# Performance work log

Measured on AMD Instinct MI355X. Metric: run time of the kernel, lower is better.

Reference implementation:

```python
import jax, jax.numpy as jnp
import numpy as np

N = 50000
E = 800000
EMB = 128
HID = 128
HALF = HID // 2

def setup_inputs() -> dict:
    key = jax.random.key(0)
    ks = jax.random.split(key, 16)
    inp = {
        "x": jax.random.normal(ks[0], (N, EMB), dtype=jnp.float32),
        "edge_row": jax.random.randint(ks[1], (E,), 0, N, dtype=jnp.int32),
        "edge_col": jax.random.randint(ks[2], (E,), 0, N, dtype=jnp.int32),
        "edge_vals": jax.random.uniform(ks[3], (E,), dtype=jnp.float32),
        "W_gc0": jax.random.normal(ks[4], (EMB, HID), dtype=jnp.float32) * 0.05,
        "b_gc0": jax.random.normal(ks[5], (HID,), dtype=jnp.float32) * 0.05,
        "W_gc1": jax.random.normal(ks[6], (HID, HID), dtype=jnp.float32) * 0.05,
        "b_gc1": jax.random.normal(ks[7], (HID,), dtype=jnp.float32) * 0.05,
        "Wm1": jax.random.normal(ks[8], (HID, HALF), dtype=jnp.float32) * 0.05,
        "bm1": jax.random.normal(ks[9], (HALF,), dtype=jnp.float32) * 0.05,
        "Wm2": jax.random.normal(ks[10], (HALF, HALF), dtype=jnp.float32) * 0.05,
        "bm2": jax.random.normal(ks[11], (HALF,), dtype=jnp.float32) * 0.05,
        "Wv1": jax.random.normal(ks[12], (HID, HALF), dtype=jnp.float32) * 0.05,
        "bv1": jax.random.normal(ks[13], (HALF,), dtype=jnp.float32) * 0.05,
        "Wv2": jax.random.normal(ks[14], (HALF, HALF), dtype=jnp.float32) * 0.05,
        "bv2": jax.random.normal(ks[15], (HALF,), dtype=jnp.float32) * 0.05,
    }
    return inp

def reference(x, edge_row, edge_col, edge_vals,
              W_gc0, b_gc0, W_gc1, b_gc1,
              Wm1, bm1, Wm2, bm2, Wv1, bv1, Wv2, bv2):
    n = x.shape[0]

    def gcn_layer(h, W, b):
        # support = h @ W  (dense GEMM), then spmm: out[r] += adj[r,c] * support[c]
        support = h @ W                                   # [N, out]
        msgs = edge_vals[:, None] * support[edge_col]      # [E, out]
        agg = jax.ops.segment_sum(msgs, edge_row, num_segments=n)
        return agg + b

    h = jax.nn.relu(gcn_layer(x, W_gc0, b_gc0))
    h = jax.nn.relu(gcn_layer(h, W_gc1, b_gc1))

    mean = jax.nn.relu(h @ Wm1 + bm1) @ Wm2 + bm2
    logvar = jax.nn.relu(h @ Wv1 + bv1) @ Wv2 + bv2
    return mean, logvar
```

## Files before the change

kernel.cpp:

```cpp
#include <hip/hip_runtime.h>
#include <type_traits>


typedef _Float16 half8 __attribute__((ext_vector_type(8)));
typedef float floatx4 __attribute__((ext_vector_type(4)));

#define BCAP 2560
#define CHUNK 2048
#define RB 128

template<int K, int M, bool RELU, bool BIAS2, bool SPLIT, typename InT, typename OutT>
__global__ __launch_bounds__(256)
void gemm16(const InT* __restrict__ A, const _Float16* __restrict__ Wswz,
            const float* __restrict__ bias0, const float* __restrict__ bias1,
            OutT* __restrict__ C0, OutT* __restrict__ C1, int n) {
  constexpr int NT = M / 16, KS = K / 32;
  const int lane = threadIdx.x & 63;
  const int wave = threadIdx.x >> 6;
  const int quad = lane >> 4, l16 = lane & 15;
  const int r_base = blockIdx.x * 128 + wave * 32;

  int arow0 = r_base + l16;
  int arow1 = r_base + 16 + l16;
  if (arow0 >= n) arow0 = n - 1;
  if (arow1 >= n) arow1 = n - 1;
  const InT* Ap0 = A + (size_t)arow0 * K + quad * 8;
  const InT* Ap1 = A + (size_t)arow1 * K + quad * 8;

  floatx4 acc[2][NT] = {};

#pragma unroll
  for (int ks = 0; ks < KS; ++ks) {
    half8 a0, a1;
    if constexpr (std::is_same_v<InT, _Float16>) {
      a0 = *(const half8*)(Ap0 + ks * 32);
      a1 = *(const half8*)(Ap1 + ks * 32);
    } else {
      float4 u = *(const float4*)(Ap0 + ks * 32);
      float4 w = *(const float4*)(Ap0 + ks * 32 + 4);
      a0 = half8{(_Float16)u.x, (_Float16)u.y, (_Float16)u.z, (_Float16)u.w,
                 (_Float16)w.x, (_Float16)w.y, (_Float16)w.z, (_Float16)w.w};
      float4 u1 = *(const float4*)(Ap1 + ks * 32);
      float4 w1 = *(const float4*)(Ap1 + ks * 32 + 4);
      a1 = half8{(_Float16)u1.x, (_Float16)u1.y, (_Float16)u1.z, (_Float16)u1.w,
                 (_Float16)w1.x, (_Float16)w1.y, (_Float16)w1.z, (_Float16)w1.w};
    }
#pragma unroll
    for (int nt = 0; nt < NT; ++nt) {
      half8 b = *(const half8*)(Wswz + ((size_t)(ks * NT + nt) * 64 + lane) * 8);
      acc[0][nt] = __builtin_amdgcn_mfma_f32_16x16x32_f16(a0, b, acc[0][nt], 0, 0, 0);
      acc[1][nt] = __builtin_amdgcn_mfma_f32_16x16x32_f16(a1, b, acc[1][nt], 0, 0, 0);
    }
  }

#pragma unroll
  for (int h = 0; h < 2; ++h) {
#pragma unroll
    for (int nt = 0; nt < NT; ++nt) {
      const int col = nt * 16 + l16;
      float bv = 0.f;
      if constexpr (BIAS2) bv = (col < 64) ? bias0[col] : bias1[col - 64];
#pragma unroll
      for (int r = 0; r < 4; ++r) {
        int row = r_base + h * 16 + quad * 4 + r;
        if (row < n) {
          float v = acc[h][nt][r] + bv;
          if constexpr (RELU) v = fmaxf(v, 0.f);
          if constexpr (SPLIT) {
            if (col < 64) C0[(size_t)row * 64 + col] = (OutT)v;
            else          C1[(size_t)row * 64 + (col - 64)] = (OutT)v;
          } else {
            C0[(size_t)row * M + col] = (OutT)v;
          }
        }
      }
    }
  }
}

__global__ __launch_bounds__(256)
void wconv_kernel(const float* __restrict__ w0, const float* __restrict__ w1,
                  const float* __restrict__ wm1, const float* __restrict__ wv1,
                  const float* __restrict__ wm2, const float* __restrict__ wv2,
                  _Float16* __restrict__ d0, _Float16* __restrict__ d1,
                  _Float16* __restrict__ dh1, _Float16* __restrict__ dh2) {
  int i = blockIdx.x * 256 + threadIdx.x;
  if (i >= 65536) return;
  int seg = i >> 14, li = i & 16383;
  int j = li & 7, lane = (li >> 3) & 63, t = li >> 9;
  int nt = t & 7, ks = t >> 3;
  int k = ks * 32 + (lane >> 4) * 8 + j;
  int n = nt * 16 + (lane & 15);
  float v;
  if (seg == 0)      v = w0[k * 128 + n];
  else if (seg == 1) v = w1[k * 128 + n];
  else if (seg == 2) v = (n < 64) ? wm1[k * 64 + n] : wv1[k * 64 + (n - 64)];
  else v = (k < 64 && n < 64) ? wm2[k * 64 + n]
         : (k >= 64 && n >= 64) ? wv2[(k - 64) * 64 + (n - 64)] : 0.f;
  _Float16* dst = (seg == 0) ? d0 : (seg == 1) ? d1 : (seg == 2) ? dh1 : dh2;
  dst[li] = (_Float16)v;
}

__global__ __launch_bounds__(256)
void blockbin_kernel(const int* __restrict__ rows, const int* __restrict__ cols,
                     const float* __restrict__ vals,
                     int* __restrict__ bcur, uint2* __restrict__ bbuf, int e) {
  __shared__ int cnt[392];
  __shared__ int cur[392];
  const int t = threadIdx.x;
  const int lo = blockIdx.x * CHUNK, hi = min(lo + CHUNK, e);
  for (int j = t; j < 392; j += 256) cnt[j] = 0;
  __syncthreads();
  for (int i = lo + t; i < hi; i += 256)
    atomicAdd(&cnt[rows[i] >> 7], 1);
  __syncthreads();
  for (int j = t; j < 392; j += 256)
    if (cnt[j] > 0) cur[j] = atomicAdd(&bcur[j * 16], cnt[j]);
  __syncthreads();
  for (int i = lo + t; i < hi; i += 256) {
    int r = rows[i];
    int b = r >> 7;
    int p = atomicAdd(&cur[b], 1);
    if (p < BCAP)
      bbuf[(size_t)b * BCAP + p] =
          make_uint2(((unsigned)(r & (RB - 1)) << 16) | (unsigned)cols[i],
                     __float_as_uint(vals[i]));
  }
}

__global__ __launch_bounds__(512)
void bscan_kernel(const int* __restrict__ bcur, int* __restrict__ bbase,
                  int* __restrict__ row_ptr, int nbk, int n) {
  __shared__ int s[512];
  int t = threadIdx.x;
  int c = (t < nbk) ? bcur[t * 16] : 0;
  s[t] = c;
  __syncthreads();
#pragma unroll
  for (int off = 1; off < 512; off <<= 1) {
    int a = (t >= off) ? s[t - off] : 0;
    __syncthreads();
    s[t] += a;
    __syncthreads();
  }
  if (t < nbk) bbase[t] = s[t] - c;
  if (t == 511) row_ptr[n] = s[511];
}

__global__ __launch_bounds__(256)
void bucketB_kernel(const uint2* __restrict__ bbuf, const int* __restrict__ bcur,
                    const int* __restrict__ bbase, int* __restrict__ row_ptr,
                    int2* __restrict__ s_pack, int n) {
  __shared__ int cnt[RB];
  __shared__ int scn[RB];
  __shared__ int2 stage[BCAP];
  const int b = blockIdx.x, t = threadIdx.x;
  const int e = min(bcur[b * 16], BCAP);
  const int base = bbase[b];
  const uint2* src = bbuf + (size_t)b * BCAP;

  if (t < RB) cnt[t] = 0;
  __syncthreads();
  for (int i = t; i < e; i += 256)
    atomicAdd(&cnt[(src[i].x >> 16) & (RB - 1)], 1);
  __syncthreads();
  int c = (t < RB) ? cnt[t] : 0;
  if (t < RB) scn[t] = c;
  __syncthreads();
#pragma unroll
  for (int off = 1; off < RB; off <<= 1) {
    int a = (t >= off && t < RB) ? scn[t - off] : 0;
    __syncthreads();
    if (t < RB) scn[t] += a;
    __syncthreads();
  }
  if (t < RB) {
    int excl = scn[t] - c;
    int grow = b * RB + t;
    if (grow < n) row_ptr[grow] = base + excl;
    cnt[t] = excl;
  }
  __syncthreads();
  for (int i = t; i < e; i += 256) {
    uint2 u = src[i];
    int pos = atomicAdd(&cnt[(u.x >> 16) & (RB - 1)], 1);
    stage[pos] = make_int2((int)(u.x & 0xFFFFu), (int)u.y);
  }
  __syncthreads();
  for (int i = t; i < e; i += 256)
    s_pack[base + i] = stage[i];
}

template<bool HEADS>
__global__ __launch_bounds__(256)
void spmm_fused(const half8* __restrict__ sup, const int* __restrict__ row_ptr,
                const int2* __restrict__ s_pack, const float* __restrict__ gbias,
                const _Float16* __restrict__ W1swz, const _Float16* __restrict__ W2swz,
                const float* __restrict__ hb0, const float* __restrict__ hb1,
                const float* __restrict__ ob0, const float* __restrict__ ob1,
                _Float16* __restrict__ outA, float* __restrict__ outM,
                float* __restrict__ outV, int n) {
  __shared__ _Float16 hs[16][136];
  __shared__ _Float16 ts[HEADS ? 16 : 1][136];
  const int t = threadIdx.x;
  const int g = t >> 4;
  const int l = t & 15;
  int r = blockIdx.x * 16 + g;
  if (r >= n) r = n - 1;
  const int beg = row_ptr[r], end = row_ptr[r + 1];

  float acc[8] = {};
  int i = beg;
  for (; i + 3 < end; i += 4) {
    int2 e0 = s_pack[i], e1 = s_pack[i + 1], e2 = s_pack[i + 2], e3 = s_pack[i + 3];
    half8 g0 = sup[(size_t)e0.x * 16 + l];
    half8 g1 = sup[(size_t)e1.x * 16 + l];
    half8 g2 = sup[(size_t)e2.x * 16 + l];
    half8 g3 = sup[(size_t)e3.x * 16 + l];
    float v0 = __int_as_float(e0.y), v1 = __int_as_float(e1.y);
    float v2 = __int_as_float(e2.y), v3 = __int_as_float(e3.y);
#pragma unroll
    for (int jj = 0; jj < 8; ++jj) acc[jj] = fmaf(v0, (float)g0[jj], acc[jj]);
#pragma unroll
    for (int jj = 0; jj < 8; ++jj) acc[jj] = fmaf(v1, (float)g1[jj], acc[jj]);
#pragma unroll
    for (int jj = 0; jj < 8; ++jj) acc[jj] = fmaf(v2, (float)g2[jj], acc[jj]);
#pragma unroll
    for (int jj = 0; jj < 8; ++jj) acc[jj] = fmaf(v3, (float)g3[jj], acc[jj]);
  }
  for (; i < end; ++i) {
    int2 e0 = s_pack[i];
    float v = __int_as_float(e0.y);
    half8 gg = sup[(size_t)e0.x * 16 + l];
#pragma unroll
    for (int jj = 0; jj < 8; ++jj) acc[jj] = fmaf(v, (float)gg[jj], acc[jj]);
  }

  float4 b0 = *(const float4*)(gbias + 8 * l);
  float4 b1 = *(const float4*)(gbias + 8 * l + 4);
  _Float16* hp = &hs[g][8 * l];
  hp[0] = (_Float16)fmaxf(acc[0] + b0.x, 0.f);
  hp[1] = (_Float16)fmaxf(acc[1] + b0.y, 0.f);
  hp[2] = (_Float16)fmaxf(acc[2] + b0.z, 0.f);
  hp[3] = (_Float16)fmaxf(acc[3] + b0.w, 0.f);
  hp[4] = (_Float16)fmaxf(acc[4] + b1.x, 0.f);
  hp[5] = (_Float16)fmaxf(acc[5] + b1.y, 0.f);
  hp[6] = (_Float16)fmaxf(acc[6] + b1.z, 0.f);
  hp[7] = (_Float16)fmaxf(acc[7] + b1.w, 0.f);
  __syncthreads();

  const int lane = t & 63, wave = t >> 6;
  const int quad = lane >> 4, l16 = lane & 15;
  floatx4 cacc[2] = {{0.f, 0.f, 0.f, 0.f}, {0.f, 0.f, 0.f, 0.f}};
#pragma unroll
  for (int ks = 0; ks < 4; ++ks) {
    half8 a = *(const half8*)&hs[l16][ks * 32 + quad * 8];
#pragma unroll
    for (int nt = 0; nt < 2; ++nt) {
      int ntg = wave * 2 + nt;
      half8 b = *(const half8*)(W1swz + ((size_t)(ks * 8 + ntg) * 64 + lane) * 8);
      cacc[nt] = __builtin_amdgcn_mfma_f32_16x16x32_f16(a, b, cacc[nt], 0, 0, 0);
    }
  }

  if constexpr (!HEADS) {
#pragma unroll
    for (int nt = 0; nt < 2; ++nt) {
      int col = wave * 32 + nt * 16 + l16;
#pragma unroll
      for (int rr = 0; rr < 4; ++rr) {
        int row = blockIdx.x * 16 + quad * 4 + rr;
        if (row < n) outA[(size_t)row * 128 + col] = (_Float16)cacc[nt][rr];
      }
    }
  } else {
#pragma unroll
    for (int nt = 0; nt < 2; ++nt) {
      int col = wave * 32 + nt * 16 + l16;
      float bv = (col < 64) ? hb0[col] : hb1[col - 64];
#pragma unroll
      for (int rr = 0; rr < 4; ++rr)
        ts[quad * 4 + rr][col] = (_Float16)fmaxf(cacc[nt][rr] + bv, 0.f);
    }
    __syncthreads();
    floatx4 oacc[2] = {{0.f, 0.f, 0.f, 0.f}, {0.f, 0.f, 0.f, 0.f}};
#pragma unroll
    for (int ks = 0; ks < 4; ++ks) {
      half8 a = *(const half8*)&ts[l16][ks * 32 + quad * 8];
#pragma unroll
      for (int nt = 0; nt < 2; ++nt) {
        int ntg = wave * 2 + nt;
        half8 b = *(const half8*)(W2swz + ((size_t)(ks * 8 + ntg) * 64 + lane) * 8);
        oacc[nt] = __builtin_amdgcn_mfma_f32_16x16x32_f16(a, b, oacc[nt], 0, 0, 0);
      }
    }
#pragma unroll
    for (int nt = 0; nt < 2; ++nt) {
      int col = wave * 32 + nt * 16 + l16;
      float bv = (col < 64) ? ob0[col] : ob1[col - 64];
#pragma unroll
      for (int rr = 0; rr < 4; ++rr) {
        int row = blockIdx.x * 16 + quad * 4 + rr;
        if (row < n) {
          float v = oacc[nt][rr] + bv;
          if (col < 64) outM[(size_t)row * 64 + col] = v;
          else          outV[(size_t)row * 64 + (col - 64)] = v;
        }
      }
    }
  }
}

extern "C" void kernel_launch(void* const* d_in, const int* in_sizes, int n_in,
                              void* d_out, int out_size, void* d_ws, size_t ws_size,
                              hipStream_t stream) {
  const float* x        = (const float*)d_in[0];
  const int*   edge_row = (const int*)d_in[1];
  const int*   edge_col = (const int*)d_in[2];
  const float* edge_val = (const float*)d_in[3];
  const float* W_gc0 = (const float*)d_in[4];
  const float* b_gc0 = (const float*)d_in[5];
  const float* W_gc1 = (const float*)d_in[6];
  const float* b_gc1 = (const float*)d_in[7];
  const float* Wm1 = (const float*)d_in[8];
  const float* bm1 = (const float*)d_in[9];
  const float* Wm2 = (const float*)d_in[10];
  const float* bm2 = (const float*)d_in[11];
  const float* Wv1 = (const float*)d_in[12];
  const float* bv1 = (const float*)d_in[13];
  const float* Wv2 = (const float*)d_in[14];
  const float* bv2 = (const float*)d_in[15];

  const int N = in_sizes[0] / 128;
  const int E = in_sizes[1];
  const int NBK = (N + RB - 1) / RB;

  char* ws = (char*)d_ws;
  _Float16* bufA16 = (_Float16*)(ws);
  _Float16* bufB16 = (_Float16*)(ws + (size_t)N * 256);
  int2*  s_pack = (int2*)(ws + (size_t)N * 512);
  char*  p = ws + (size_t)N * 512 + (size_t)E * 8;
  int*   row_ptr = (int*)p;           p += 200064;
  int*   bcur    = (int*)p;           p += (size_t)NBK * 64;
  int*   bbase   = (int*)p;           p += 2048;
  uint2* bbuf    = (uint2*)p;         p += (size_t)NBK * BCAP * 8;
  _Float16* W0s  = (_Float16*)p;      p += 32768;
  _Float16* W1s  = (_Float16*)p;      p += 32768;
  _Float16* Wh1s = (_Float16*)p;      p += 32768;
  _Float16* Wh2s = (_Float16*)p;      p += 32768;

  float* out_mean = (float*)d_out;
  float* out_lvar = out_mean + (size_t)N * 64;

  hipMemsetAsync(bcur, 0, (size_t)NBK * 64, stream);
  blockbin_kernel<<<(E + CHUNK - 1) / CHUNK, 256, 0, stream>>>(edge_row, edge_col, edge_val,
                                                               bcur, bbuf, E);
  bscan_kernel<<<1, 512, 0, stream>>>(bcur, bbase, row_ptr, NBK, N);
  bucketB_kernel<<<NBK, 256, 0, stream>>>(bbuf, bcur, bbase, row_ptr, s_pack, N);
  wconv_kernel<<<256, 256, 0, stream>>>(W_gc0, W_gc1, Wm1, Wv1, Wm2, Wv2,
                                        W0s, W1s, Wh1s, Wh2s);

  const int GB = (N + 127) / 128;
  const int SB = (N + 15) / 16;

  gemm16<128, 128, false, false, false, float, _Float16>
      <<<GB, 256, 0, stream>>>(x, W0s, nullptr, nullptr, bufA16, nullptr, N);
  spmm_fused<false><<<SB, 256, 0, stream>>>((const half8*)bufA16, row_ptr, s_pack,
                                            b_gc0, W1s, nullptr,
                                            nullptr, nullptr, nullptr, nullptr,
                                            bufB16, nullptr, nullptr, N);
  spmm_fused<true><<<SB, 256, 0, stream>>>((const half8*)bufB16, row_ptr, s_pack,
                                           b_gc1, Wh1s, Wh2s,
                                           bm1, bv1, bm2, bv2,
                                           nullptr, out_mean, out_lvar, N);
}
```

Baseline: 218.9 us.

## Group rows by degree via counting sort so SpMM blocks have balanced work

Builds a degree histogram in bucketB, scans it in a new tiny kernel, and counting-sorts row indices into a degree-ordered permutation inside the weight-conversion launch. Both SpMM kernels then process rows in that order and write results back through the permutation. This aims to cut the divergence that arises when 16 rows of very different degree share a block. In exchange it adds an extra kernel launch, an extra indirection per row, and scattered output writes.

```diff
diff --git a/kernel.cpp b/kernel.cpp
--- a/kernel.cpp
+++ b/kernel.cpp
@@ -83,20 +83,42 @@
                   const float* __restrict__ wm1, const float* __restrict__ wv1,
                   const float* __restrict__ wm2, const float* __restrict__ wv2,
                   _Float16* __restrict__ d0, _Float16* __restrict__ d1,
-                  _Float16* __restrict__ dh1, _Float16* __restrict__ dh2) {
-  int i = blockIdx.x * 256 + threadIdx.x;
+                  _Float16* __restrict__ dh1, _Float16* __restrict__ dh2,
+                  const int* __restrict__ row_ptr, int* __restrict__ gcur,
+                  int* __restrict__ rperm, int n) {
+  __shared__ int lh[64];
+  __shared__ int lbase[64];
+  const int t = threadIdx.x;
+  if (blockIdx.x >= 256) {
+    const int rb = (blockIdx.x - 256) * RB;
+    if (t < 64) lh[t] = 0;
+    __syncthreads();
+    int myidx = 0, bin = 0, r = rb + t;
+    bool valid = (t < RB) && (r < n);
+    if (valid) {
+      int deg = row_ptr[r + 1] - row_ptr[r];
+      bin = min(deg, 63);
+      myidx = atomicAdd(&lh[bin], 1);
+    }
+    __syncthreads();
+    if (t < 64 && lh[t] > 0) lbase[t] = atomicAdd(&gcur[t], lh[t]);
+    __syncthreads();
+    if (valid) rperm[lbase[bin] + myidx] = r;
+    return;
+  }
+  int i = blockIdx.x * 256 + t;
   if (i >= 65536) return;
   int seg = i >> 14, li = i & 16383;
-  int j = li & 7, lane = (li >> 3) & 63, t = li >> 9;
-  int nt = t & 7, ks = t >> 3;
+  int j = li & 7, lane = (li >> 3) & 63, tt = li >> 9;
+  int nt = tt & 7, ks = tt >> 3;
   int k = ks * 32 + (lane >> 4) * 8 + j;
-  int n = nt * 16 + (lane & 15);
+  int nn = nt * 16 + (lane & 15);
   float v;
-  if (seg == 0)      v = w0[k * 128 + n];
-  else if (seg == 1) v = w1[k * 128 + n];
-  else if (seg == 2) v = (n < 64) ? wm1[k * 64 + n] : wv1[k * 64 + (n - 64)];
-  else v = (k < 64 && n < 64) ? wm2[k * 64 + n]
-         : (k >= 64 && n >= 64) ? wv2[(k - 64) * 64 + (n - 64)] : 0.f;
+  if (seg == 0)      v = w0[k * 128 + nn];
+  else if (seg == 1) v = w1[k * 128 + nn];
+  else if (seg == 2) v = (nn < 64) ? wm1[k * 64 + nn] : wv1[k * 64 + (nn - 64)];
+  else v = (k < 64 && nn < 64) ? wm2[k * 64 + nn]
+         : (k >= 64 && nn >= 64) ? wv2[(k - 64) * 64 + (nn - 64)] : 0.f;
   _Float16* dst = (seg == 0) ? d0 : (seg == 1) ? d1 : (seg == 2) ? dh1 : dh2;
   dst[li] = (_Float16)v;
 }
@@ -150,9 +172,10 @@
 __global__ __launch_bounds__(256)
 void bucketB_kernel(const uint2* __restrict__ bbuf, const int* __restrict__ bcur,
                     const int* __restrict__ bbase, int* __restrict__ row_ptr,
-                    int2* __restrict__ s_pack, int n) {
+                    int2* __restrict__ s_pack, int* __restrict__ ghist, int n) {
   __shared__ int cnt[RB];
   __shared__ int scn[RB];
+  __shared__ int lh[64];
   __shared__ int2 stage[BCAP];
   const int b = blockIdx.x, t = threadIdx.x;
   const int e = min(bcur[b * 16], BCAP);
@@ -160,6 +183,7 @@
   const uint2* src = bbuf + (size_t)b * BCAP;
 
   if (t < RB) cnt[t] = 0;
+  if (t >= RB && t < RB + 64) lh[t - RB] = 0;
   __syncthreads();
   for (int i = t; i < e; i += 256)
     atomicAdd(&cnt[(src[i].x >> 16) & (RB - 1)], 1);
@@ -177,10 +201,14 @@
   if (t < RB) {
     int excl = scn[t] - c;
     int grow = b * RB + t;
-    if (grow < n) row_ptr[grow] = base + excl;
+    if (grow < n) {
+      row_ptr[grow] = base + excl;
+      atomicAdd(&lh[min(c, 63)], 1);
+    }
     cnt[t] = excl;
   }
   __syncthreads();
+  if (t < 64 && lh[t] > 0) atomicAdd(&ghist[t], lh[t]);
   for (int i = t; i < e; i += 256) {
     uint2 u = src[i];
     int pos = atomicAdd(&cnt[(u.x >> 16) & (RB - 1)], 1);
@@ -191,10 +219,22 @@
     s_pack[base + i] = stage[i];
 }
 
+__global__ __launch_bounds__(64)
+void degscan_kernel(const int* __restrict__ ghist, int* __restrict__ gcur) {
+  __shared__ int s[64];
+  int t = threadIdx.x;
+  s[t] = ghist[t];
+  __syncthreads();
+  int acc = 0;
+  for (int j = 0; j < t; ++j) acc += s[j];
+  gcur[t] = acc;
+}
+
 template<bool HEADS>
 __global__ __launch_bounds__(256)
 void spmm_fused(const half8* __restrict__ sup, const int* __restrict__ row_ptr,
                 const int2* __restrict__ s_pack, const float* __restrict__ gbias,
+                const int* __restrict__ rperm,
                 const _Float16* __restrict__ W1swz, const _Float16* __restrict__ W2swz,
                 const float* __restrict__ hb0, const float* __restrict__ hb1,
                 const float* __restrict__ ob0, const float* __restrict__ ob1,
@@ -202,11 +242,14 @@
                 float* __restrict__ outV, int n) {
   __shared__ _Float16 hs[16][136];
   __shared__ _Float16 ts[HEADS ? 16 : 1][136];
+  __shared__ int rs[16];
   const int t = threadIdx.x;
   const int g = t >> 4;
   const int l = t & 15;
-  int r = blockIdx.x * 16 + g;
-  if (r >= n) r = n - 1;
+  int ridx = blockIdx.x * 16 + g;
+  if (ridx >= n) ridx = n - 1;
+  const int r = rperm[ridx];
+  if (l == 0) rs[g] = r;
   const int beg = row_ptr[r], end = row_ptr[r + 1];
 
   float acc[8] = {};
@@ -269,8 +312,9 @@
       int col = wave * 32 + nt * 16 + l16;
 #pragma unroll
       for (int rr = 0; rr < 4; ++rr) {
-        int row = blockIdx.x * 16 + quad * 4 + rr;
-        if (row < n) outA[(size_t)row * 128 + col] = (_Float16)cacc[nt][rr];
+        int slot = quad * 4 + rr;
+        if (blockIdx.x * 16 + slot < n)
+          outA[(size_t)rs[slot] * 128 + col] = (_Float16)cacc[nt][rr];
       }
     }
   } else {
@@ -300,11 +344,12 @@
       float bv = (col < 64) ? ob0[col] : ob1[col - 64];
 #pragma unroll
       for (int rr = 0; rr < 4; ++rr) {
-        int row = blockIdx.x * 16 + quad * 4 + rr;
-        if (row < n) {
+        int slot = quad * 4 + rr;
+        if (blockIdx.x * 16 + slot < n) {
           float v = oacc[nt][rr] + bv;
-          if (col < 64) outM[(size_t)row * 64 + col] = v;
-          else          outV[(size_t)row * 64 + (col - 64)] = v;
+          int orow = rs[slot];
+          if (col < 64) outM[(size_t)orow * 64 + col] = v;
+          else          outV[(size_t)orow * 64 + (col - 64)] = v;
         }
       }
     }
@@ -342,7 +387,10 @@
   char*  p = ws + (size_t)N * 512 + (size_t)E * 8;
   int*   row_ptr = (int*)p;           p += 200064;
   int*   bcur    = (int*)p;           p += (size_t)NBK * 64;
+  int*   ghist   = (int*)p;           p += 256;
+  int*   gcur    = (int*)p;           p += 256;
   int*   bbase   = (int*)p;           p += 2048;
+  int*   rperm   = (int*)p;           p += (size_t)N * 4;
   uint2* bbuf    = (uint2*)p;         p += (size_t)NBK * BCAP * 8;
   _Float16* W0s  = (_Float16*)p;      p += 32768;
   _Float16* W1s  = (_Float16*)p;      p += 32768;
@@ -352,13 +400,15 @@
   float* out_mean = (float*)d_out;
   float* out_lvar = out_mean + (size_t)N * 64;
 
-  hipMemsetAsync(bcur, 0, (size_t)NBK * 64, stream);
+  hipMemsetAsync(bcur, 0, (size_t)NBK * 64 + 512, stream);
   blockbin_kernel<<<(E + CHUNK - 1) / CHUNK, 256, 0, stream>>>(edge_row, edge_col, edge_val,
                                                                bcur, bbuf, E);
   bscan_kernel<<<1, 512, 0, stream>>>(bcur, bbase, row_ptr, NBK, N);
-  bucketB_kernel<<<NBK, 256, 0, stream>>>(bbuf, bcur, bbase, row_ptr, s_pack, N);
-  wconv_kernel<<<256, 256, 0, stream>>>(W_gc0, W_gc1, Wm1, Wv1, Wm2, Wv2,
-                                        W0s, W1s, Wh1s, Wh2s);
+  bucketB_kernel<<<NBK, 256, 0, stream>>>(bbuf, bcur, bbase, row_ptr, s_pack, ghist, N);
+  degscan_kernel<<<1, 64, 0, stream>>>(ghist, gcur);
+  wconv_kernel<<<256 + NBK, 256, 0, stream>>>(W_gc0, W_gc1, Wm1, Wv1, Wm2, Wv2,
+                                              W0s, W1s, Wh1s, Wh2s,
+                                              row_ptr, gcur, rperm, N);
 
   const int GB = (N + 127) / 128;
   const int SB = (N + 15) / 16;
@@ -366,11 +416,11 @@
   gemm16<128, 128, false, false, false, float, _Float16>
       <<<GB, 256, 0, stream>>>(x, W0s, nullptr, nullptr, bufA16, nullptr, N);
   spmm_fused<false><<<SB, 256, 0, stream>>>((const half8*)bufA16, row_ptr, s_pack,
-                                            b_gc0, W1s, nullptr,
+                                            b_gc0, rperm, W1s, nullptr,
                                             nullptr, nullptr, nullptr, nullptr,
                                             bufB16, nullptr, nullptr, N);
   spmm_fused<true><<<SB, 256, 0, stream>>>((const half8*)bufB16, row_ptr, s_pack,
-                                           b_gc1, Wh1s, Wh2s,
+                                           b_gc1, rperm, Wh1s, Wh2s,
                                            bm1, bv1, bm2, bv2,
                                            nullptr, out_mean, out_lvar, N);
 }
```

After: 232.6 us. 6.3% more time.

## Merge independent preprocessing kernels into shared launches with block-range dispatch

Applied to the files above, without the earlier changes.

Folds weight conversion into the edge-binning kernel and the layer-0 dense GEMM into the bucket-sort kernel, selecting the role by block index. This cuts two kernel launches and lets independent work run concurrently on otherwise idle CUs. The cost is that the GEMM blocks now carry the bucket kernel's large shared-memory allocation, which may reduce occupancy. The GEMM still runs after the weight conversion it depends on.

```diff
diff --git a/kernel.cpp b/kernel.cpp
--- a/kernel.cpp
+++ b/kernel.cpp
@@ -9,45 +9,36 @@
 #define CHUNK 2048
 #define RB 128
 
-template<int K, int M, bool RELU, bool BIAS2, bool SPLIT, typename InT, typename OutT>
-__global__ __launch_bounds__(256)
-void gemm16(const InT* __restrict__ A, const _Float16* __restrict__ Wswz,
-            const float* __restrict__ bias0, const float* __restrict__ bias1,
-            OutT* __restrict__ C0, OutT* __restrict__ C1, int n) {
-  constexpr int NT = M / 16, KS = K / 32;
-  const int lane = threadIdx.x & 63;
-  const int wave = threadIdx.x >> 6;
+__device__ void gemm_l1(int bid, const float* __restrict__ A,
+                        const _Float16* __restrict__ Wswz,
+                        _Float16* __restrict__ C0, int n) {
+  const int t = threadIdx.x;
+  const int lane = t & 63, wave = t >> 6;
   const int quad = lane >> 4, l16 = lane & 15;
-  const int r_base = blockIdx.x * 128 + wave * 32;
+  const int r_base = bid * 128 + wave * 32;
 
   int arow0 = r_base + l16;
   int arow1 = r_base + 16 + l16;
   if (arow0 >= n) arow0 = n - 1;
   if (arow1 >= n) arow1 = n - 1;
-  const InT* Ap0 = A + (size_t)arow0 * K + quad * 8;
-  const InT* Ap1 = A + (size_t)arow1 * K + quad * 8;
-
-  floatx4 acc[2][NT] = {};
-
-#pragma unroll
-  for (int ks = 0; ks < KS; ++ks) {
-    half8 a0, a1;
-    if constexpr (std::is_same_v<InT, _Float16>) {
-      a0 = *(const half8*)(Ap0 + ks * 32);
-      a1 = *(const half8*)(Ap1 + ks * 32);
-    } else {
-      float4 u = *(const float4*)(Ap0 + ks * 32);
-      float4 w = *(const float4*)(Ap0 + ks * 32 + 4);
-      a0 = half8{(_Float16)u.x, (_Float16)u.y, (_Float16)u.z, (_Float16)u.w,
-                 (_Float16)w.x, (_Float16)w.y, (_Float16)w.z, (_Float16)w.w};
-      float4 u1 = *(const float4*)(Ap1 + ks * 32);
-      float4 w1 = *(const float4*)(Ap1 + ks * 32 + 4);
-      a1 = half8{(_Float16)u1.x, (_Float16)u1.y, (_Float16)u1.z, (_Float16)u1.w,
-                 (_Float16)w1.x, (_Float16)w1.y, (_Float16)w1.z, (_Float16)w1.w};
-    }
-#pragma unroll
-    for (int nt = 0; nt < NT; ++nt) {
-      half8 b = *(const half8*)(Wswz + ((size_t)(ks * NT + nt) * 64 + lane) * 8);
+  const float* Ap0 = A + (size_t)arow0 * 128 + quad * 8;
+  const float* Ap1 = A + (size_t)arow1 * 128 + quad * 8;
+
+  floatx4 acc[2][8] = {};
+
+#pragma unroll
+  for (int ks = 0; ks < 4; ++ks) {
+    float4 u = *(const float4*)(Ap0 + ks * 32);
+    float4 w = *(const float4*)(Ap0 + ks * 32 + 4);
+    half8 a0 = half8{(_Float16)u.x, (_Float16)u.y, (_Float16)u.z, (_Float16)u.w,
+                     (_Float16)w.x, (_Float16)w.y, (_Float16)w.z, (_Float16)w.w};
+    float4 u1 = *(const float4*)(Ap1 + ks * 32);
+    float4 w1 = *(const float4*)(Ap1 + ks * 32 + 4);
+    half8 a1 = half8{(_Float16)u1.x, (_Float16)u1.y, (_Float16)u1.z, (_Float16)u1.w,
+                     (_Float16)w1.x, (_Float16)w1.y, (_Float16)w1.z, (_Float16)w1.w};
+#pragma unroll
+    for (int nt = 0; nt < 8; ++nt) {
+      half8 b = *(const half8*)(Wswz + ((size_t)(ks * 8 + nt) * 64 + lane) * 8);
       acc[0][nt] = __builtin_amdgcn_mfma_f32_16x16x32_f16(a0, b, acc[0][nt], 0, 0, 0);
       acc[1][nt] = __builtin_amdgcn_mfma_f32_16x16x32_f16(a1, b, acc[1][nt], 0, 0, 0);
     }
@@ -56,58 +47,50 @@
 #pragma unroll
   for (int h = 0; h < 2; ++h) {
 #pragma unroll
-    for (int nt = 0; nt < NT; ++nt) {
+    for (int nt = 0; nt < 8; ++nt) {
       const int col = nt * 16 + l16;
-      float bv = 0.f;
-      if constexpr (BIAS2) bv = (col < 64) ? bias0[col] : bias1[col - 64];
 #pragma unroll
       for (int r = 0; r < 4; ++r) {
         int row = r_base + h * 16 + quad * 4 + r;
-        if (row < n) {
-          float v = acc[h][nt][r] + bv;
-          if constexpr (RELU) v = fmaxf(v, 0.f);
-          if constexpr (SPLIT) {
-            if (col < 64) C0[(size_t)row * 64 + col] = (OutT)v;
-            else          C1[(size_t)row * 64 + (col - 64)] = (OutT)v;
-          } else {
-            C0[(size_t)row * M + col] = (OutT)v;
-          }
-        }
+        if (row < n) C0[(size_t)row * 128 + col] = (_Float16)acc[h][nt][r];
       }
     }
   }
 }
 
 __global__ __launch_bounds__(256)
-void wconv_kernel(const float* __restrict__ w0, const float* __restrict__ w1,
-                  const float* __restrict__ wm1, const float* __restrict__ wv1,
-                  const float* __restrict__ wm2, const float* __restrict__ wv2,
-                  _Float16* __restrict__ d0, _Float16* __restrict__ d1,
-                  _Float16* __restrict__ dh1, _Float16* __restrict__ dh2) {
-  int i = blockIdx.x * 256 + threadIdx.x;
-  if (i >= 65536) return;
-  int seg = i >> 14, li = i & 16383;
-  int j = li & 7, lane = (li >> 3) & 63, t = li >> 9;
-  int nt = t & 7, ks = t >> 3;
-  int k = ks * 32 + (lane >> 4) * 8 + j;
-  int n = nt * 16 + (lane & 15);
-  float v;
-  if (seg == 0)      v = w0[k * 128 + n];
-  else if (seg == 1) v = w1[k * 128 + n];
-  else if (seg == 2) v = (n < 64) ? wm1[k * 64 + n] : wv1[k * 64 + (n - 64)];
-  else v = (k < 64 && n < 64) ? wm2[k * 64 + n]
-         : (k >= 64 && n >= 64) ? wv2[(k - 64) * 64 + (n - 64)] : 0.f;
-  _Float16* dst = (seg == 0) ? d0 : (seg == 1) ? d1 : (seg == 2) ? dh1 : dh2;
-  dst[li] = (_Float16)v;
-}
-
-__global__ __launch_bounds__(256)
-void blockbin_kernel(const int* __restrict__ rows, const int* __restrict__ cols,
-                     const float* __restrict__ vals,
-                     int* __restrict__ bcur, uint2* __restrict__ bbuf, int e) {
+void buildA_kernel(const int* __restrict__ rows, const int* __restrict__ cols,
+                   const float* __restrict__ vals,
+                   int* __restrict__ bcur, uint2* __restrict__ bbuf, int e,
+                   int binBlocks,
+                   const float* __restrict__ w0, const float* __restrict__ w1,
+                   const float* __restrict__ wm1, const float* __restrict__ wv1,
+                   const float* __restrict__ wm2, const float* __restrict__ wv2,
+                   _Float16* __restrict__ d0, _Float16* __restrict__ d1,
+                   _Float16* __restrict__ dh1, _Float16* __restrict__ dh2) {
   __shared__ int cnt[392];
   __shared__ int cur[392];
   const int t = threadIdx.x;
+
+  if (blockIdx.x >= binBlocks) {
+    int i = (blockIdx.x - binBlocks) * 256 + t;
+    if (i >= 65536) return;
+    int seg = i >> 14, li = i & 16383;
+    int j = li & 7, lane = (li >> 3) & 63, tt = li >> 9;
+    int nt = tt & 7, ks = tt >> 3;
+    int k = ks * 32 + (lane >> 4) * 8 + j;
+    int nn = nt * 16 + (lane & 15);
+    float v;
+    if (seg == 0)      v = w0[k * 128 + nn];
+    else if (seg == 1) v = w1[k * 128 + nn];
+    else if (seg == 2) v = (nn < 64) ? wm1[k * 64 + nn] : wv1[k * 64 + (nn - 64)];
+    else v = (k < 64 && nn < 64) ? wm2[k * 64 + nn]
+           : (k >= 64 && nn >= 64) ? wv2[(k - 64) * 64 + (nn - 64)] : 0.f;
+    _Float16* dst = (seg == 0) ? d0 : (seg == 1) ? d1 : (seg == 2) ? dh1 : dh2;
+    dst[li] = (_Float16)v;
+    return;
+  }
+
   const int lo = blockIdx.x * CHUNK, hi = min(lo + CHUNK, e);
   for (int j = t; j < 392; j += 256) cnt[j] = 0;
   __syncthreads();
@@ -148,12 +131,20 @@
 }
 
 __global__ __launch_bounds__(256)
-void bucketB_kernel(const uint2* __restrict__ bbuf, const int* __restrict__ bcur,
-                    const int* __restrict__ bbase, int* __restrict__ row_ptr,
-                    int2* __restrict__ s_pack, int n) {
+void buildB_kernel(const uint2* __restrict__ bbuf, const int* __restrict__ bcur,
+                   const int* __restrict__ bbase, int* __restrict__ row_ptr,
+                   int2* __restrict__ s_pack, int nbk, int n,
+                   const float* __restrict__ x, const _Float16* __restrict__ W0s,
+                   _Float16* __restrict__ sup) {
   __shared__ int cnt[RB];
   __shared__ int scn[RB];
   __shared__ int2 stage[BCAP];
+
+  if (blockIdx.x >= nbk) {
+    gemm_l1(blockIdx.x - nbk, x, W0s, sup, n);
+    return;
+  }
+
   const int b = blockIdx.x, t = threadIdx.x;
   const int e = min(bcur[b * 16], BCAP);
   const int base = bbase[b];
@@ -353,18 +344,17 @@
   float* out_lvar = out_mean + (size_t)N * 64;
 
   hipMemsetAsync(bcur, 0, (size_t)NBK * 64, stream);
-  blockbin_kernel<<<(E + CHUNK - 1) / CHUNK, 256, 0, stream>>>(edge_row, edge_col, edge_val,
-                                                               bcur, bbuf, E);
+  const int binBlocks = (E + CHUNK - 1) / CHUNK;
+  buildA_kernel<<<binBlocks + 256, 256, 0, stream>>>(
+      edge_row, edge_col, edge_val, bcur, bbuf, E, binBlocks,
+      W_gc0, W_gc1, Wm1, Wv1, Wm2, Wv2, W0s, W1s, Wh1s, Wh2s);
   bscan_kernel<<<1, 512, 0, stream>>>(bcur, bbase, row_ptr, NBK, N);
-  bucketB_kernel<<<NBK, 256, 0, stream>>>(bbuf, bcur, bbase, row_ptr, s_pack, N);
-  wconv_kernel<<<256, 256, 0, stream>>>(W_gc0, W_gc1, Wm1, Wv1, Wm2, Wv2,
-                                        W0s, W1s, Wh1s, Wh2s);
 
   const int GB = (N + 127) / 128;
   const int SB = (N + 15) / 16;
 
-  gemm16<128, 128, false, false, false, float, _Float16>
-      <<<GB, 256, 0, stream>>>(x, W0s, nullptr, nullptr, bufA16, nullptr, N);
+  buildB_kernel<<<NBK + GB, 256, 0, stream>>>(bbuf, bcur, bbase, row_ptr, s_pack,
+                                              NBK, N, x, W0s, bufA16);
   spmm_fused<false><<<SB, 256, 0, stream>>>((const half8*)bufA16, row_ptr, s_pack,
                                             b_gc0, W1s, nullptr,
                                             nullptr, nullptr, nullptr, nullptr,
```

Measured after the change: 212.8 us. 1.03x faster.
